# Optimization experiments

Measured on AMD Instinct MI355X. Metric: run time of the kernel, lower is better.

Reference implementation:

```python
import jax, jax.numpy as jnp
import numpy as np

U = 128  # LSTM units (hardcoded in module)


def _lstm(x_tm, W, Urec, b, return_sequences):
    """Keras-style LSTM. x_tm: [T,B,F] time-major. Gate order i,f,c(g),o.
    activation=tanh, recurrent_activation=sigmoid. recurrent_dropout is
    inference-mode identity (dropout only active in training)."""
    T, B, _ = x_tm.shape
    xz = jnp.einsum('tbf,fg->tbg', x_tm, W) + b  # precompute input projections [T,B,4U]

    def step(carry, xz_t):
        h, c = carry
        z = xz_t + h @ Urec  # [B,4U]
        i, f, g, o = jnp.split(z, 4, axis=-1)
        i = jax.nn.sigmoid(i)
        f = jax.nn.sigmoid(f)
        g = jnp.tanh(g)
        o = jax.nn.sigmoid(o)
        c_new = f * c + i * g
        h_new = o * jnp.tanh(c_new)
        return (h_new, c_new), h_new

    h0 = jnp.zeros((B, U), x_tm.dtype)
    c0 = jnp.zeros((B, U), x_tm.dtype)
    (h_last, _), hs = jax.lax.scan(step, (h0, c0), xz)
    return hs if return_sequences else h_last


def setup_inputs() -> dict:
    key = jax.random.key(0)
    ks = jax.random.split(key, 7)
    B, T, F = 512, 256, 64
    s_in = 1.0 / np.sqrt(F)
    s_rec = 1.0 / np.sqrt(U)
    return {
        'x': jax.random.normal(ks[0], (B, T, F), jnp.float32),
        'W1': jax.random.normal(ks[1], (F, 4 * U), jnp.float32) * s_in,
        'U1': jax.random.normal(ks[2], (U, 4 * U), jnp.float32) * s_rec,
        'b1': jnp.zeros((4 * U,), jnp.float32),
        'W2': jax.random.normal(ks[3], (U, 4 * U), jnp.float32) * s_rec,
        'U2': jax.random.normal(ks[4], (U, 4 * U), jnp.float32) * s_rec,
        'b2': jnp.zeros((4 * U,), jnp.float32),
        'Wd': jax.random.normal(ks[5], (U, 1), jnp.float32) * s_rec,
        'bd': jnp.zeros((1,), jnp.float32),
    }


def reference(x, W1, U1, b1, W2, U2, b2, Wd, bd):
    x_tm = jnp.transpose(x, (1, 0, 2))  # [T,B,F]
    hs = _lstm(x_tm, W1, U1, b1, return_sequences=True)   # hidden_lstm -> [T,B,U]
    h_last = _lstm(hs, W2, U2, b2, return_sequences=False)  # lstm_layer -> [B,U]
    return jax.nn.relu(h_last @ Wd + bd)  # Dense(1, relu) -> [B,1]
```

## Files before the change

kernel.cpp:

```cpp
#include <hip/hip_runtime.h>


#define T_STEPS 256
#define BATCH   512
#define NU      128
#define FDIM    64

typedef _Float16 h8 __attribute__((ext_vector_type(8)));
typedef _Float16 h4 __attribute__((ext_vector_type(4)));
typedef float    f4 __attribute__((ext_vector_type(4)));

#define LOG2E    1.4426950408889634f
#define TWOLOG2E 2.8853900817779268f

#define WG_BARRIER() asm volatile("s_waitcnt lgkmcnt(0)\n\ts_barrier" ::: "memory")

#if __has_builtin(__builtin_amdgcn_exp2f)
#define EXP2F(x) __builtin_amdgcn_exp2f(x)
#else
#define EXP2F(x) exp2f(x)
#endif
#if __has_builtin(__builtin_amdgcn_rcpf)
#define RCPF(x) __builtin_amdgcn_rcpf(x)
#else
#define RCPF(x) (1.0f / (x))
#endif

__device__ __forceinline__ float sigm2(float s) {
    return RCPF(1.0f + EXP2F(s));
}
__device__ __forceinline__ float tanh2(float t) {
    return 1.0f - 2.0f * RCPF(1.0f + EXP2F(t));
}

__global__ void prep_weights(const float* __restrict__ W1, const float* __restrict__ U1,
                             const float* __restrict__ b1, const float* __restrict__ W2,
                             const float* __restrict__ U2, const float* __restrict__ b2,
                             _Float16* __restrict__ Wp1, _Float16* __restrict__ Up1,
                             _Float16* __restrict__ Wp2, _Float16* __restrict__ Up2,
                             float* __restrict__ bp1, float* __restrict__ bp2) {
    int i = blockIdx.x * 256 + threadIdx.x;
    if (i < 32768) {
        int col = i >> 6, k = i & 63;
        float sc = ((col >> 7) == 2) ? TWOLOG2E : -LOG2E;
        Wp1[i] = (_Float16)(W1[k * 512 + col] * sc);
    } else if (i < 32768 + 65536) {
        int j = i - 32768; int col = j >> 7, k = j & 127;
        float sc = ((col >> 7) == 2) ? TWOLOG2E : -LOG2E;
        Up1[j] = (_Float16)(U1[k * 512 + col] * sc);
    } else if (i < 32768 + 131072) {
        int j = i - 98304; int col = j >> 7, k = j & 127;
        float sc = ((col >> 7) == 2) ? TWOLOG2E : -LOG2E;
        Wp2[j] = (_Float16)(W2[k * 512 + col] * sc);
    } else if (i < 32768 + 196608) {
        int j = i - 163840; int col = j >> 7, k = j & 127;
        float sc = ((col >> 7) == 2) ? TWOLOG2E : -LOG2E;
        Up2[j] = (_Float16)(U2[k * 512 + col] * sc);
    } else if (i < 32768 + 196608 + 1024) {
        int j = i - 229376;
        if (j < 512) {
            float sc = ((j >> 7) == 2) ? TWOLOG2E : -LOG2E;
            bp1[j] = b1[j] * sc;
        } else {
            int col = j - 512;
            float sc = ((col >> 7) == 2) ? TWOLOG2E : -LOG2E;
            bp2[col] = b2[col] * sc;
        }
    }
}

template <bool IS_A>
__attribute__((amdgpu_waves_per_eu(2, 2)))
__global__ __launch_bounds__(512) void lstm_layer(
    const float* __restrict__ xA, const _Float16* __restrict__ xB,
    const _Float16* __restrict__ Wp,
    const _Float16* __restrict__ Up,
    const float* __restrict__ bp,
    _Float16* __restrict__ hs_out,
    const float* __restrict__ Wd, const float* __restrict__ bd,
    float* __restrict__ dout) {
    constexpr int KX  = IS_A ? 64 : 128;
    constexpr int KXS = KX / 32;
    constexpr int PH  = 136;
    constexpr int H0  = 0;
    constexpr int H1  = 2 * PH;

    __shared__ __align__(16) _Float16 smh[4 * PH];
    __shared__ __align__(16) float smxz[2 * 8 * 128 * 2 * 4];

    const int tid  = threadIdx.x;
    const int lane = tid & 63;
    const int wv   = tid >> 6;
    const int m    = lane & 15;
    const int kc   = lane >> 4;
    const int u0   = wv * 16;
    const int b0   = blockIdx.x * 2;

    for (int i = tid; i < 4 * PH; i += 512) smh[i] = (_Float16)0.0f;

    h8 uf[4][4];
#pragma unroll
    for (int g = 0; g < 4; g++)
#pragma unroll
        for (int ks = 0; ks < 4; ks++)
            uf[g][ks] = *(const h8*)&Up[(g * 128 + u0 + m) * 128 + ks * 32 + kc * 8];
    h8 wf[4][KXS];
#pragma unroll
    for (int g = 0; g < 4; g++)
#pragma unroll
        for (int ks = 0; ks < KXS; ks++)
            wf[g][ks] = *(const h8*)&Wp[(g * 128 + u0 + m) * KX + ks * 32 + kc * 8];
    float bias[4];
#pragma unroll
    for (int g = 0; g < 4; g++) bias[g] = bp[g * 128 + u0 + m];

    f4 rX[4]; h8 rH[4];
    auto loadA = [&](int kblk) {
        int tt = kblk * 8 + (m >> 1); if (tt > T_STEPS - 1) tt = T_STEPS - 1;
        const int bb = b0 + (m & 1);
        if constexpr (IS_A) {
#pragma unroll
            for (int ks = 0; ks < KXS; ks++)
#pragma unroll
                for (int hf = 0; hf < 2; hf++)
                    rX[ks * 2 + hf] = *(const f4*)&xA[((size_t)bb * T_STEPS + tt) * FDIM
                                                      + ks * 32 + kc * 8 + hf * 4];
        } else {
#pragma unroll
            for (int ks = 0; ks < 4; ks++)
                rH[ks] = *(const h8*)&xB[((size_t)tt * BATCH + bb) * NU + ks * 32 + kc * 8];
        }
    };
    auto calcX = [&](int kblk) {
        float* xzw = &smxz[(kblk & 1) * 8192];
        f4 accx[4];
#pragma unroll
        for (int g = 0; g < 4; g++) accx[g] = (f4){bias[g], bias[g], bias[g], bias[g]};
#pragma unroll
        for (int ks = 0; ks < KXS; ks++) {
            h8 a;
            if constexpr (IS_A) {
#pragma unroll
                for (int j = 0; j < 4; j++) {
                    a[j]     = (_Float16)rX[ks * 2][j];
                    a[4 + j] = (_Float16)rX[ks * 2 + 1][j];
                }
            } else {
                a = rH[ks];
            }
#pragma unroll
            for (int g = 0; g < 4; g++)
                accx[g] = __builtin_amdgcn_mfma_f32_16x16x32_f16(a, wf[g][ks], accx[g], 0, 0, 0);
        }
#pragma unroll
        for (int g = 0; g < 4; g++)
#pragma unroll
            for (int rr = 0; rr < 4; rr++) {
                int r16 = kc * 4 + rr;
                xzw[(((r16 >> 1) * 128 + u0 + m) * 2 + (r16 & 1)) * 4 + g] = accx[g][rr];
            }
    };

    loadA(0); calcX(0);
    loadA(1);
    __syncthreads();

    const h8 hzero = {};
    h8 ha[4];
#pragma unroll
    for (int ks = 0; ks < 4; ks++) ha[ks] = hzero;

    const int erow = lane >> 4;
    float cst = 0.0f;

#pragma unroll 8
    for (int t = 0; t < T_STEPS; t++) {
        const int p = t & 1;
        const int s = t & 7;

        if (s == 0) {
            int kn = (t >> 3) + 1;
            if (kn < T_STEPS / 8) {
                calcX(kn);
                loadA(kn + 1);
            }
        }

        if (m == 0 || m == 4) {
            const _Float16* hb = &smh[(p ? H1 : H0) + (m == 4 ? PH : 0)];
#pragma unroll
            for (int ks = 0; ks < 4; ks++)
                ha[ks] = *(const h8*)&hb[ks * 32 + kc * 8];
        }

        f4 acc[4];
#pragma unroll
        for (int g = 0; g < 4; g++) acc[g] = (f4){0.f, 0.f, 0.f, 0.f};
#pragma unroll
        for (int ks = 0; ks < 4; ks++)
#pragma unroll
            for (int g = 0; g < 4; g++)
                acc[g] = __builtin_amdgcn_mfma_f32_16x16x32_f16(ha[ks], uf[g][ks], acc[g], 0, 0, 0);

        if (lane < 32) {
            const f4 xzv = *(const f4*)&smxz[((t >> 3) & 1) * 8192
                                             + ((s * 128 + u0 + m) * 2 + erow) * 4];
            float gi = sigm2(acc[0][0] + xzv[0]);
            float gf = sigm2(acc[1][0] + xzv[1]);
            float gg = tanh2(acc[2][0] + xzv[2]);
            float go = sigm2(acc[3][0] + xzv[3]);
            cst = gf * cst + gi * gg;
            float hv = go * tanh2(cst * TWOLOG2E);
            _Float16 h16 = (_Float16)hv;
            smh[(p ? H0 : H1) + erow * PH + u0 + m] = h16;
            if constexpr (IS_A)
                hs_out[((size_t)t * BATCH + b0 + erow) * NU + u0 + m] = h16;
        }
        WG_BARRIER();
    }

    if constexpr (!IS_A) {
        if (wv == 0) {
            int rw = lane >> 5, u = lane & 31;
            float sacc = 0.0f;
#pragma unroll
            for (int j = 0; j < 4; j++) {
                int uum = u + j * 32;
                sacc += (float)smh[H0 + rw * PH + uum] * Wd[uum];
            }
            sacc += __shfl_xor(sacc, 16);
            sacc += __shfl_xor(sacc, 8);
            sacc += __shfl_xor(sacc, 4);
            sacc += __shfl_xor(sacc, 2);
            sacc += __shfl_xor(sacc, 1);
            if ((lane & 31) == 0) dout[b0 + rw] = fmaxf(sacc + bd[0], 0.0f);
        }
    }
}

extern "C" void kernel_launch(void* const* d_in, const int* in_sizes, int n_in,
                              void* d_out, int out_size, void* d_ws, size_t ws_size,
                              hipStream_t stream) {
    const float* x  = (const float*)d_in[0];
    const float* W1 = (const float*)d_in[1];
    const float* U1 = (const float*)d_in[2];
    const float* b1 = (const float*)d_in[3];
    const float* W2 = (const float*)d_in[4];
    const float* U2 = (const float*)d_in[5];
    const float* b2 = (const float*)d_in[6];
    const float* Wd = (const float*)d_in[7];
    const float* bd = (const float*)d_in[8];
    float* out = (float*)d_out;

    const size_t HS   = 33554432;
    const size_t oWp1 = HS;
    const size_t oUp1 = oWp1 + 65536;
    const size_t oWp2 = oUp1 + 131072;
    const size_t oUp2 = oWp2 + 131072;
    const size_t oBp1 = oUp2 + 131072;
    const size_t oBp2 = oBp1 + 2048;
    const size_t need = oBp2 + 2048;
    if (ws_size < need) return;

    char* ws = (char*)d_ws;
    _Float16* hs  = (_Float16*)ws;
    _Float16* Wp1 = (_Float16*)(ws + oWp1);
    _Float16* Up1 = (_Float16*)(ws + oUp1);
    _Float16* Wp2 = (_Float16*)(ws + oWp2);
    _Float16* Up2 = (_Float16*)(ws + oUp2);
    float*    bp1 = (float*)(ws + oBp1);
    float*    bp2 = (float*)(ws + oBp2);

    prep_weights<<<900, 256, 0, stream>>>(W1, U1, b1, W2, U2, b2,
                                          Wp1, Up1, Wp2, Up2, bp1, bp2);
    lstm_layer<true><<<256, 512, 0, stream>>>(x, nullptr, Wp1, Up1, bp1,
                                              hs, nullptr, nullptr, nullptr);
    lstm_layer<false><<<256, 512, 0, stream>>>(nullptr, hs, Wp2, Up2, bp2,
                                               nullptr, Wd, bd, out);
}
```

Measured before the change: 358.2 us.

## Fuse both LSTM layers into one wavefront-skewed kernel, keep hidden states in LDS

Merges the two per-layer kernels into a single kernel where layer 2 runs one 8-step block behind layer 1. Layer-1 hidden states stay in a 16-step LDS ring instead of going through a global hs buffer. Each timestep runs both recurrent MFMA chains: lanes 0-31 update layer 1 and lanes 32-63 update layer 2. This removes the 32 MB global round trip and the serial second recurrence, at the cost of more registers (both U matrices held), larger LDS, 8 extra steps, and W1/W2 reloaded from global each block.

```diff
diff --git a/kernel.cpp b/kernel.cpp
--- a/kernel.cpp
+++ b/kernel.cpp
@@ -5,9 +5,9 @@
 #define BATCH   512
 #define NU      128
 #define FDIM    64
+#define PH      136
 
 typedef _Float16 h8 __attribute__((ext_vector_type(8)));
-typedef _Float16 h4 __attribute__((ext_vector_type(4)));
 typedef float    f4 __attribute__((ext_vector_type(4)));
 
 #define LOG2E    1.4426950408889634f
@@ -44,19 +44,19 @@
         int col = i >> 6, k = i & 63;
         float sc = ((col >> 7) == 2) ? TWOLOG2E : -LOG2E;
         Wp1[i] = (_Float16)(W1[k * 512 + col] * sc);
-    } else if (i < 32768 + 65536) {
+    } else if (i < 98304) {
         int j = i - 32768; int col = j >> 7, k = j & 127;
         float sc = ((col >> 7) == 2) ? TWOLOG2E : -LOG2E;
         Up1[j] = (_Float16)(U1[k * 512 + col] * sc);
-    } else if (i < 32768 + 131072) {
+    } else if (i < 163840) {
         int j = i - 98304; int col = j >> 7, k = j & 127;
         float sc = ((col >> 7) == 2) ? TWOLOG2E : -LOG2E;
         Wp2[j] = (_Float16)(W2[k * 512 + col] * sc);
-    } else if (i < 32768 + 196608) {
+    } else if (i < 229376) {
         int j = i - 163840; int col = j >> 7, k = j & 127;
         float sc = ((col >> 7) == 2) ? TWOLOG2E : -LOG2E;
         Up2[j] = (_Float16)(U2[k * 512 + col] * sc);
-    } else if (i < 32768 + 196608 + 1024) {
+    } else if (i < 230400) {
         int j = i - 229376;
         if (j < 512) {
             float sc = ((j >> 7) == 2) ? TWOLOG2E : -LOG2E;
@@ -69,24 +69,21 @@
     }
 }
 
-template <bool IS_A>
 __attribute__((amdgpu_waves_per_eu(2, 2)))
-__global__ __launch_bounds__(512) void lstm_layer(
-    const float* __restrict__ xA, const _Float16* __restrict__ xB,
-    const _Float16* __restrict__ Wp,
-    const _Float16* __restrict__ Up,
-    const float* __restrict__ bp,
-    _Float16* __restrict__ hs_out,
+__global__ __launch_bounds__(512) void lstm_fused(
+    const float* __restrict__ x,
+    const _Float16* __restrict__ Wp1, const _Float16* __restrict__ Up1,
+    const float* __restrict__ bp1,
+    const _Float16* __restrict__ Wp2, const _Float16* __restrict__ Up2,
+    const float* __restrict__ bp2,
     const float* __restrict__ Wd, const float* __restrict__ bd,
     float* __restrict__ dout) {
-    constexpr int KX  = IS_A ? 64 : 128;
-    constexpr int KXS = KX / 32;
-    constexpr int PH  = 136;
-    constexpr int H0  = 0;
-    constexpr int H1  = 2 * PH;
-
-    __shared__ __align__(16) _Float16 smh[4 * PH];
-    __shared__ __align__(16) float smxz[2 * 8 * 128 * 2 * 4];
+    __shared__ __align__(16) _Float16 smh[(32 + 4) * PH];
+    __shared__ __align__(16) float smxz[32768];
+    _Float16* h1r = smh;
+    _Float16* h2r = smh + 32 * PH;
+    float* xz1 = smxz;
+    float* xz2 = smxz + 16384;
 
     const int tid  = threadIdx.x;
     const int lane = tid & 63;
@@ -95,146 +92,156 @@
     const int kc   = lane >> 4;
     const int u0   = wv * 16;
     const int b0   = blockIdx.x * 2;
-
-    for (int i = tid; i < 4 * PH; i += 512) smh[i] = (_Float16)0.0f;
-
-    h8 uf[4][4];
+    const int erow = (lane >> 4) & 1;
+
+    for (int i = tid; i < 36 * PH; i += 512) smh[i] = (_Float16)0.0f;
+    for (int i = tid; i < 32768; i += 512) smxz[i] = 0.0f;
+
+    h8 uf1[4][4], uf2[4][4];
 #pragma unroll
     for (int g = 0; g < 4; g++)
 #pragma unroll
-        for (int ks = 0; ks < 4; ks++)
-            uf[g][ks] = *(const h8*)&Up[(g * 128 + u0 + m) * 128 + ks * 32 + kc * 8];
-    h8 wf[4][KXS];
-#pragma unroll
-    for (int g = 0; g < 4; g++)
-#pragma unroll
-        for (int ks = 0; ks < KXS; ks++)
-            wf[g][ks] = *(const h8*)&Wp[(g * 128 + u0 + m) * KX + ks * 32 + kc * 8];
-    float bias[4];
-#pragma unroll
-    for (int g = 0; g < 4; g++) bias[g] = bp[g * 128 + u0 + m];
-
-    f4 rX[4]; h8 rH[4];
-    auto loadA = [&](int kblk) {
-        int tt = kblk * 8 + (m >> 1); if (tt > T_STEPS - 1) tt = T_STEPS - 1;
-        const int bb = b0 + (m & 1);
-        if constexpr (IS_A) {
-#pragma unroll
-            for (int ks = 0; ks < KXS; ks++)
-#pragma unroll
-                for (int hf = 0; hf < 2; hf++)
-                    rX[ks * 2 + hf] = *(const f4*)&xA[((size_t)bb * T_STEPS + tt) * FDIM
-                                                      + ks * 32 + kc * 8 + hf * 4];
-        } else {
+        for (int ks = 0; ks < 4; ks++) {
+            uf1[g][ks] = *(const h8*)&Up1[(g * 128 + u0 + m) * 128 + ks * 32 + kc * 8];
+            uf2[g][ks] = *(const h8*)&Up2[(g * 128 + u0 + m) * 128 + ks * 32 + kc * 8];
+        }
+    float b1v[4], b2v[4];
+#pragma unroll
+    for (int g = 0; g < 4; g++) {
+        b1v[g] = bp1[g * 128 + u0 + m];
+        b2v[g] = bp2[g * 128 + u0 + m];
+    }
+
+    __syncthreads();
+
+    const h8 hz = {};
+    h8 ha[4];
+#pragma unroll
+    for (int ks = 0; ks < 4; ks++) ha[ks] = hz;
+    f4 fz = (f4){0.f, 0.f, 0.f, 0.f};
+    asm volatile("" : "+v"(fz));
+    float cst = 0.0f;
+
+#pragma unroll 8
+    for (int t = 0; t < T_STEPS + 8; t++) {
+        const int s = t & 7;
+        const int b = t >> 3;
+
+        if (s == 0) {
+            if (b < 32) {
+                const int tt = b * 8 + (m >> 1), bb = b0 + (m & 1);
+                const float* xp = &x[((size_t)bb * T_STEPS + tt) * FDIM];
+                f4 x0 = *(const f4*)&xp[kc * 8];
+                f4 x1 = *(const f4*)&xp[kc * 8 + 4];
+                f4 x2 = *(const f4*)&xp[32 + kc * 8];
+                f4 x3 = *(const f4*)&xp[32 + kc * 8 + 4];
+                h8 a0, a1;
+#pragma unroll
+                for (int j = 0; j < 4; j++) {
+                    a0[j] = (_Float16)x0[j]; a0[4 + j] = (_Float16)x1[j];
+                    a1[j] = (_Float16)x2[j]; a1[4 + j] = (_Float16)x3[j];
+                }
+                f4 ax[4];
+#pragma unroll
+                for (int g = 0; g < 4; g++) {
+                    ax[g] = (f4){b1v[g], b1v[g], b1v[g], b1v[g]};
+                    h8 w0 = *(const h8*)&Wp1[(g * 128 + u0 + m) * 64 + kc * 8];
+                    h8 w1 = *(const h8*)&Wp1[(g * 128 + u0 + m) * 64 + 32 + kc * 8];
+                    ax[g] = __builtin_amdgcn_mfma_f32_16x16x32_f16(a0, w0, ax[g], 0, 0, 0);
+                    ax[g] = __builtin_amdgcn_mfma_f32_16x16x32_f16(a1, w1, ax[g], 0, 0, 0);
+                }
+                float* dstz = &xz1[(b & 1) * 8192];
+#pragma unroll
+                for (int rr = 0; rr < 4; rr++) {
+                    f4 v = {ax[0][rr], ax[1][rr], ax[2][rr], ax[3][rr]};
+                    *(f4*)&dstz[((kc * 4 + rr) * 128 + u0 + m) * 4] = v;
+                }
+            }
+            if (b >= 1 && b < 33) {
+                const int b2 = b - 1, hh = b2 & 1;
+                const _Float16* hp = &h1r[((hh * 8 + (m >> 1)) * 2 + (m & 1)) * PH];
+                h8 a[4];
+#pragma unroll
+                for (int ks = 0; ks < 4; ks++)
+                    a[ks] = *(const h8*)&hp[ks * 32 + kc * 8];
+                f4 ax[4];
+#pragma unroll
+                for (int g = 0; g < 4; g++)
+                    ax[g] = (f4){b2v[g], b2v[g], b2v[g], b2v[g]};
+#pragma unroll
+                for (int ks = 0; ks < 4; ks++)
+#pragma unroll
+                    for (int g = 0; g < 4; g++) {
+                        h8 w = *(const h8*)&Wp2[(g * 128 + u0 + m) * 128 + ks * 32 + kc * 8];
+                        ax[g] = __builtin_amdgcn_mfma_f32_16x16x32_f16(a[ks], w, ax[g], 0, 0, 0);
+                    }
+                float* dstz = &xz2[hh * 8192];
+#pragma unroll
+                for (int rr = 0; rr < 4; rr++) {
+                    f4 v = {ax[0][rr], ax[1][rr], ax[2][rr], ax[3][rr]};
+                    *(f4*)&dstz[((kc * 4 + rr) * 128 + u0 + m) * 4] = v;
+                }
+            }
+            WG_BARRIER();
+        }
+
+        if ((m & 3) == 0) {
+            const _Float16* src = (m < 8)
+                ? &h1r[(((t - 1) & 15) * 2 + (m >> 2)) * PH]
+                : &h2r[((t & 1) * 2 + ((m >> 2) - 2)) * PH];
 #pragma unroll
             for (int ks = 0; ks < 4; ks++)
-                rH[ks] = *(const h8*)&xB[((size_t)tt * BATCH + bb) * NU + ks * 32 + kc * 8];
-        }
-    };
-    auto calcX = [&](int kblk) {
-        float* xzw = &smxz[(kblk & 1) * 8192];
-        f4 accx[4];
-#pragma unroll
-        for (int g = 0; g < 4; g++) accx[g] = (f4){bias[g], bias[g], bias[g], bias[g]};
-#pragma unroll
-        for (int ks = 0; ks < KXS; ks++) {
-            h8 a;
-            if constexpr (IS_A) {
-#pragma unroll
-                for (int j = 0; j < 4; j++) {
-                    a[j]     = (_Float16)rX[ks * 2][j];
-                    a[4 + j] = (_Float16)rX[ks * 2 + 1][j];
-                }
-            } else {
-                a = rH[ks];
+                ha[ks] = *(const h8*)&src[ks * 32 + kc * 8];
+        }
+
+        f4 ac1[4], ac2[4];
+#pragma unroll
+        for (int g = 0; g < 4; g++) {
+            ac1[g] = __builtin_amdgcn_mfma_f32_16x16x32_f16(ha[0], uf1[g][0], fz, 0, 0, 0);
+            ac2[g] = __builtin_amdgcn_mfma_f32_16x16x32_f16(ha[0], uf2[g][0], fz, 0, 0, 0);
+        }
+#pragma unroll
+        for (int ks = 1; ks < 4; ks++)
+#pragma unroll
+            for (int g = 0; g < 4; g++) {
+                ac1[g] = __builtin_amdgcn_mfma_f32_16x16x32_f16(ha[ks], uf1[g][ks], ac1[g], 0, 0, 0);
+                ac2[g] = __builtin_amdgcn_mfma_f32_16x16x32_f16(ha[ks], uf2[g][ks], ac2[g], 0, 0, 0);
             }
-#pragma unroll
-            for (int g = 0; g < 4; g++)
-                accx[g] = __builtin_amdgcn_mfma_f32_16x16x32_f16(a, wf[g][ks], accx[g], 0, 0, 0);
-        }
-#pragma unroll
-        for (int g = 0; g < 4; g++)
-#pragma unroll
-            for (int rr = 0; rr < 4; rr++) {
-                int r16 = kc * 4 + rr;
-                xzw[(((r16 >> 1) * 128 + u0 + m) * 2 + (r16 & 1)) * 4 + g] = accx[g][rr];
-            }
-    };
-
-    loadA(0); calcX(0);
-    loadA(1);
-    __syncthreads();
-
-    const h8 hzero = {};
-    h8 ha[4];
-#pragma unroll
-    for (int ks = 0; ks < 4; ks++) ha[ks] = hzero;
-
-    const int erow = lane >> 4;
-    float cst = 0.0f;
-
-#pragma unroll 8
-    for (int t = 0; t < T_STEPS; t++) {
-        const int p = t & 1;
-        const int s = t & 7;
-
-        if (s == 0) {
-            int kn = (t >> 3) + 1;
-            if (kn < T_STEPS / 8) {
-                calcX(kn);
-                loadA(kn + 1);
-            }
-        }
-
-        if (m == 0 || m == 4) {
-            const _Float16* hb = &smh[(p ? H1 : H0) + (m == 4 ? PH : 0)];
-#pragma unroll
-            for (int ks = 0; ks < 4; ks++)
-                ha[ks] = *(const h8*)&hb[ks * 32 + kc * 8];
-        }
-
-        f4 acc[4];
-#pragma unroll
-        for (int g = 0; g < 4; g++) acc[g] = (f4){0.f, 0.f, 0.f, 0.f};
-#pragma unroll
-        for (int ks = 0; ks < 4; ks++)
-#pragma unroll
-            for (int g = 0; g < 4; g++)
-                acc[g] = __builtin_amdgcn_mfma_f32_16x16x32_f16(ha[ks], uf[g][ks], acc[g], 0, 0, 0);
-
-        if (lane < 32) {
-            const f4 xzv = *(const f4*)&smxz[((t >> 3) & 1) * 8192
-                                             + ((s * 128 + u0 + m) * 2 + erow) * 4];
-            float gi = sigm2(acc[0][0] + xzv[0]);
-            float gf = sigm2(acc[1][0] + xzv[1]);
-            float gg = tanh2(acc[2][0] + xzv[2]);
-            float go = sigm2(acc[3][0] + xzv[3]);
+
+        {
+            const bool l1 = (lane < 32);
+            const float* xb = l1 ? &xz1[(b & 1) * 8192]
+                                 : &xz2[((b - 1) & 1) * 8192];
+            f4 xzv = *(const f4*)&xb[((s * 2 + erow) * 128 + u0 + m) * 4];
+            float z0 = (l1 ? ac1[0][0] : ac2[0][0]) + xzv[0];
+            float z1 = (l1 ? ac1[1][0] : ac2[1][0]) + xzv[1];
+            float z2 = (l1 ? ac1[2][0] : ac2[2][0]) + xzv[2];
+            float z3 = (l1 ? ac1[3][0] : ac2[3][0]) + xzv[3];
+            float gi = sigm2(z0), gf = sigm2(z1);
+            float gg = tanh2(z2), go = sigm2(z3);
             cst = gf * cst + gi * gg;
             float hv = go * tanh2(cst * TWOLOG2E);
             _Float16 h16 = (_Float16)hv;
-            smh[(p ? H0 : H1) + erow * PH + u0 + m] = h16;
-            if constexpr (IS_A)
-                hs_out[((size_t)t * BATCH + b0 + erow) * NU + u0 + m] = h16;
+            _Float16* dst = l1
+                ? &h1r[((t & 15) * 2 + erow) * PH + u0 + m]
+                : &h2r[(((t & 1) ^ 1) * 2 + erow) * PH + u0 + m];
+            *dst = h16;
         }
         WG_BARRIER();
     }
 
-    if constexpr (!IS_A) {
-        if (wv == 0) {
-            int rw = lane >> 5, u = lane & 31;
-            float sacc = 0.0f;
-#pragma unroll
-            for (int j = 0; j < 4; j++) {
-                int uum = u + j * 32;
-                sacc += (float)smh[H0 + rw * PH + uum] * Wd[uum];
-            }
-            sacc += __shfl_xor(sacc, 16);
-            sacc += __shfl_xor(sacc, 8);
-            sacc += __shfl_xor(sacc, 4);
-            sacc += __shfl_xor(sacc, 2);
-            sacc += __shfl_xor(sacc, 1);
-            if ((lane & 31) == 0) dout[b0 + rw] = fmaxf(sacc + bd[0], 0.0f);
-        }
+    if (wv == 0 && lane < 32) {
+        const int rw = lane >> 4, u = lane & 15;
+        const _Float16* hb = &h2r[rw * PH];
+        float sa = 0.0f;
+#pragma unroll
+        for (int j = 0; j < 8; j++)
+            sa += (float)hb[u + 16 * j] * Wd[u + 16 * j];
+        sa += __shfl_xor(sa, 1);
+        sa += __shfl_xor(sa, 2);
+        sa += __shfl_xor(sa, 4);
+        sa += __shfl_xor(sa, 8);
+        if (u == 0) dout[b0 + rw] = fmaxf(sa + bd[0], 0.0f);
     }
 }
 
@@ -252,18 +259,16 @@
     const float* bd = (const float*)d_in[8];
     float* out = (float*)d_out;
 
-    const size_t HS   = 33554432;
-    const size_t oWp1 = HS;
-    const size_t oUp1 = oWp1 + 65536;
-    const size_t oWp2 = oUp1 + 131072;
-    const size_t oUp2 = oWp2 + 131072;
-    const size_t oBp1 = oUp2 + 131072;
-    const size_t oBp2 = oBp1 + 2048;
-    const size_t need = oBp2 + 2048;
+    const size_t oWp1 = 0;
+    const size_t oUp1 = 65536;
+    const size_t oWp2 = 196608;
+    const size_t oUp2 = 327680;
+    const size_t oBp1 = 458752;
+    const size_t oBp2 = 460800;
+    const size_t need = 462848;
     if (ws_size < need) return;
 
     char* ws = (char*)d_ws;
-    _Float16* hs  = (_Float16*)ws;
     _Float16* Wp1 = (_Float16*)(ws + oWp1);
     _Float16* Up1 = (_Float16*)(ws + oUp1);
     _Float16* Wp2 = (_Float16*)(ws + oWp2);
@@ -273,8 +278,6 @@
 
     prep_weights<<<900, 256, 0, stream>>>(W1, U1, b1, W2, U2, b2,
                                           Wp1, Up1, Wp2, Up2, bp1, bp2);
-    lstm_layer<true><<<256, 512, 0, stream>>>(x, nullptr, Wp1, Up1, bp1,
-                                              hs, nullptr, nullptr, nullptr);
-    lstm_layer<false><<<256, 512, 0, stream>>>(nullptr, hs, Wp2, Up2, bp2,
-                                               nullptr, Wd, bd, out);
-}
+    lstm_fused<<<256, 512, 0, stream>>>(x, Wp1, Up1, bp1, Wp2, Up2, bp2,
+                                        Wd, bd, out);
+}
```

Result: slower. 522.0 us (+45.7%).
